# Performance work log

Measured on AMD Instinct MI355X. Metric: run time of the kernel, lower is better.

## Reference

```python
import jax, jax.numpy as jnp
import numpy as np

K = 4  # knn_graph(k=4, loop=False) hard-coded in H2GCN.forward


def _knn_2hop_adj(Fet, k):
    """Per-batch kNN graph -> symmetrize -> 2-hop binary adjacency [B,N,N].

    Matches create_adj + get_2hop_neighbors: edge direction and the row
    normalization in create_adj are irrelevant because get_2hop_neighbors
    symmetrizes (adj[row,col]=adj[col,row]=1) and thresholds (adj@adj > 0).
    """
    B, N, _ = Fet.shape
    sq = jnp.sum(Fet * Fet, axis=-1)  # [B,N]
    dist = sq[:, :, None] + sq[:, None, :] - 2.0 * jnp.einsum('bnf,bmf->bnm', Fet, Fet)
    eye = jnp.eye(N, dtype=bool)
    dist = jnp.where(eye[None], jnp.inf, dist)  # loop=False: exclude self
    _, idx = jax.lax.top_k(-dist, k)  # [B,N,k] nearest-neighbor indices
    b_idx = jnp.arange(B)[:, None, None]
    n_idx = jnp.arange(N)[None, :, None]
    A = jnp.zeros((B, N, N), Fet.dtype).at[b_idx, n_idx, idx].set(1.0)
    A = jnp.maximum(A, jnp.swapaxes(A, 1, 2))  # symmetrize 1-hop
    A2 = jnp.einsum('bnm,bmk->bnk', A, A)      # 2-hop counts
    A2 = jnp.where(eye[None], 0.0, A2)          # fill_diagonal_(0)
    return (A2 > 0).astype(Fet.dtype)


def _h2gcn_conv(x, A2, w1, b1, w2, b2):
    """H2GCNConv on dense binary adjacency.

    Dense matmul with binary A2 == gather(x[col]) -> fc2 -> index_add over rows;
    A2.sum(-1) == bincount(row). Degree clamped to >= 1.
    """
    ego = jnp.einsum('bnf,of->bno', x, w1) + b1   # fc1(x)
    msg = jnp.einsum('bnf,of->bno', x, w2) + b2   # fc2(x)
    agg = jnp.einsum('bnm,bmo->bno', A2, msg)     # scatter-add of neighbor msgs
    deg = jnp.maximum(jnp.sum(A2, axis=-1, keepdims=True), 1.0)
    return jax.nn.relu(jnp.concatenate([ego, agg / deg], axis=-1))


def setup_inputs() -> dict:
    key = jax.random.key(0)
    ks = jax.random.split(key, 8)
    B, N, F, NH, NC = 128, 197, 768, 512, 1000
    s = 0.02
    return {
        'Fet': jax.random.normal(ks[0], (B, N, F), jnp.float32),
        'w1_0': jax.random.normal(ks[1], (NH, F), jnp.float32) * s,
        'b1_0': jnp.zeros((NH,), jnp.float32),
        'w2_0': jax.random.normal(ks[2], (NH, F), jnp.float32) * s,
        'b2_0': jnp.zeros((NH,), jnp.float32),
        'w1_1': jax.random.normal(ks[3], (NH, 2 * NH), jnp.float32) * s,
        'b1_1': jnp.zeros((NH,), jnp.float32),
        'w2_1': jax.random.normal(ks[4], (NH, 2 * NH), jnp.float32) * s,
        'b2_1': jnp.zeros((NH,), jnp.float32),
        'fc1_w': jax.random.normal(ks[5], (NH, 4 * NH), jnp.float32) * s,
        'fc1_b': jnp.zeros((NH,), jnp.float32),
        'fc2_w': jax.random.normal(ks[6], (NC, NH), jnp.float32) * s,
        'fc2_b': jnp.zeros((NC,), jnp.float32),
    }


def reference(Fet, w1_0, b1_0, w2_0, b2_0, w1_1, b1_1, w2_1, b2_1,
              fc1_w, fc1_b, fc2_w, fc2_b):
    A2 = _knn_2hop_adj(Fet, K)
    h1 = _h2gcn_conv(Fet, A2, w1_0, b1_0, w2_0, b2_0)   # [B,N,2*nhid]
    h2 = _h2gcn_conv(h1, A2, w1_1, b1_1, w2_1, b2_1)    # [B,N,2*nhid]
    h = jnp.concatenate([h1, h2], axis=-1)              # [B,N,final_dim]
    graph_features = jnp.mean(h, axis=1)                # global_mean_pool
    p = jax.nn.relu(graph_features @ fc1_w.T + fc1_b)   # dropout is identity (eval)
    out = p @ fc2_w.T + fc2_b
    return (out, graph_features)
```

## Files before the change

kernel.cpp:

```cpp
#include <hip/hip_runtime.h>
#include <hip/hip_bf16.h>
#include <math.h>

typedef __attribute__((ext_vector_type(8))) short bf16x8;
typedef __attribute__((ext_vector_type(4))) float f32x4;

#define B_ 128
#define N_ 197
#define F_ 768
#define NH_ 512
#define D2_ 1024
#define D4_ 2048
#define NC_ 1000
#define ROWS_ (B_ * N_)
#define KA_ 224
#define NA_ 256

#define OFF_DIST0  0ull
#define OFF_SQ     19871232ull
#define OFF_ABITS  19972352ull
#define OFF_DEG    20779520ull
#define OFF_FETHI  20880640ull
#define OFF_MSGT   59710720ull
#define OFF_H1     89070848ull
#define OFF_FETLO  OFF_MSGT
#define OFF_POOL   140844288ull
#define OFF_P      141892864ull
#define OFF_WC1    142155008ull
#define OFF_WC2    143727872ull
#define OFF_DIST1  145825024ull

__device__ __forceinline__ void gll16(const void* g, void* l) {
  __builtin_amdgcn_global_load_lds((const __attribute__((address_space(1))) void*)g,
                                   (__attribute__((address_space(3))) void*)l, 16, 0, 0);
}

__device__ __forceinline__ int slot_of(int row) { return (row & 3) ^ ((row >> 2) & 3); }

__global__ __launch_bounds__(256) void cast_bf16_kernel(const float* __restrict__ src,
                                                        __hip_bfloat16* __restrict__ dst,
                                                        int n4) {
  int i = blockIdx.x * 256 + threadIdx.x;
  if (i >= n4) return;
  float4 v = ((const float4*)src)[i];
  union { __hip_bfloat16 h[4]; uint2 u; } pk;
  pk.h[0] = __float2bfloat16(v.x);
  pk.h[1] = __float2bfloat16(v.y);
  pk.h[2] = __float2bfloat16(v.z);
  pk.h[3] = __float2bfloat16(v.w);
  ((uint2*)dst)[i] = pk.u;
}

__global__ __launch_bounds__(256) void cast_hilo_sq(const float* __restrict__ X,
                                                    __hip_bfloat16* __restrict__ hi,
                                                    __hip_bfloat16* __restrict__ lo,
                                                    float* __restrict__ sq) {
  int row = blockIdx.x * 4 + (threadIdx.x >> 6);
  int lane = threadIdx.x & 63;
  const float4* xp = (const float4*)(X + (size_t)row * F_);
  uint2* hp = (uint2*)(hi + (size_t)row * F_);
  uint2* lp = (uint2*)(lo + (size_t)row * F_);
  float s = 0.f;
#pragma unroll
  for (int i = 0; i < 3; i++) {
    float4 v = xp[lane + i * 64];
    s += v.x * v.x + v.y * v.y + v.z * v.z + v.w * v.w;
    float f[4] = {v.x, v.y, v.z, v.w};
    union { __hip_bfloat16 h[4]; uint2 u; } ph, pl;
#pragma unroll
    for (int k = 0; k < 4; k++) {
      __hip_bfloat16 h = __float2bfloat16(f[k]);
      ph.h[k] = h;
      pl.h[k] = __float2bfloat16(f[k] - __bfloat162float(h));
    }
    hp[lane + i * 64] = ph.u;
    lp[lane + i * 64] = pl.u;
  }
#pragma unroll
  for (int o = 32; o > 0; o >>= 1) s += __shfl_down(s, o);
  if (lane == 0) sq[row] = s;
}

__global__ __launch_bounds__(256) void mfma_gram(const __hip_bfloat16* __restrict__ Xhi,
                                                 const __hip_bfloat16* __restrict__ Xlo,
                                                 float* __restrict__ g0,
                                                 float* __restrict__ g1) {
  __shared__ short AsH[4096];
  __shared__ short BsH[4096];
  __shared__ short AsL[4096];
  __shared__ short BsL[4096];
  const int t = threadIdx.x;
  const int wgid = blockIdx.x;
  const int L = (wgid & 7) * 96 + (wgid >> 3);
  const int b = L / 6;
  const int rbx = L - b * 6;
  const int bx = rbx % 3;
  const int khalf = rbx / 3;
  const int m0 = (bx == 0) ? 0 : 128;
  const int o0 = (bx == 2) ? 128 : 0;
  const bool mirror = (bx == 1);
  const int l = t & 63, w = t >> 6;
  const int wm = (w >> 1) * 64, wn = (w & 1) * 64;
  const int frow = l & 15, fch = l >> 4;
  const int srow = t >> 2, sslot = t & 3;
  const size_t rowbase = (size_t)b * N_;
  const char* AhiB = (const char*)(Xhi + (rowbase + m0) * F_);
  const char* AloB = (const char*)(Xlo + (rowbase + m0) * F_);
  const char* BhiB = (const char*)(Xhi + (rowbase + o0) * F_);
  const char* BloB = (const char*)(Xlo + (rowbase + o0) * F_);
  const int rb = F_ * 2;
  char* AsHB = (char*)AsH;
  char* BsHB = (char*)BsH;
  char* AsLB = (char*)AsL;
  char* BsLB = (char*)BsL;
  float* go = khalf ? g1 : g0;
  f32x4 zero = {0.f, 0.f, 0.f, 0.f};
  f32x4 acc[4][4];
#pragma unroll
  for (int i = 0; i < 4; i++)
#pragma unroll
    for (int j = 0; j < 4; j++) acc[i][j] = zero;
  const int kt0 = khalf * 12;
  for (int kt = kt0; kt < kt0 + 12; kt++) {
    const int kb = kt * 64;
#pragma unroll
    for (int u = 0; u < 2; u++) {
      int grow = u * 64 + srow;
      int gslot = sslot ^ slot_of(grow);
      size_t goff = (size_t)grow * rb + kb + gslot * 16;
      gll16(AhiB + goff, AsHB + u * 4096 + t * 16);
      gll16(BhiB + goff, BsHB + u * 4096 + t * 16);
      gll16(AloB + goff, AsLB + u * 4096 + t * 16);
      gll16(BloB + goff, BsLB + u * 4096 + t * 16);
    }
    __syncthreads();
    bf16x8 ah[4], al[4], bh[4], bl[4];
#pragma unroll
    for (int i = 0; i < 4; i++) {
      int ar = wm + i * 16 + frow;
      int aoff = ar * 64 + ((fch ^ slot_of(ar)) * 16);
      ah[i] = *(const bf16x8*)(AsHB + aoff);
      al[i] = *(const bf16x8*)(AsLB + aoff);
      int br = wn + i * 16 + frow;
      int boff = br * 64 + ((fch ^ slot_of(br)) * 16);
      bh[i] = *(const bf16x8*)(BsHB + boff);
      bl[i] = *(const bf16x8*)(BsLB + boff);
    }
#pragma unroll
    for (int i = 0; i < 4; i++)
#pragma unroll
      for (int j = 0; j < 4; j++) {
        acc[i][j] = __builtin_amdgcn_mfma_f32_16x16x32_bf16(ah[i], bh[j], acc[i][j], 0, 0, 0);
        acc[i][j] = __builtin_amdgcn_mfma_f32_16x16x32_bf16(ah[i], bl[j], acc[i][j], 0, 0, 0);
        acc[i][j] = __builtin_amdgcn_mfma_f32_16x16x32_bf16(al[i], bh[j], acc[i][j], 0, 0, 0);
      }
    __syncthreads();
  }
#pragma unroll
  for (int j = 0; j < 4; j++) {
    int m = o0 + wn + j * 16 + frow;
    if (m >= N_) continue;
#pragma unroll
    for (int i = 0; i < 4; i++) {
      int nb = m0 + wm + i * 16 + fch * 4;
#pragma unroll
      for (int r = 0; r < 4; r++) {
        int n = nb + r;
        if (n >= N_) continue;
        float g = acc[i][j][r];
        go[(rowbase + n) * N_ + m] = g;
        if (mirror) go[(rowbase + m) * N_ + n] = g;
      }
    }
  }
}

__global__ __launch_bounds__(256) void topk_kernel(const float* __restrict__ g0,
                                                   const float* __restrict__ g1,
                                                   const float* __restrict__ sq,
                                                   unsigned long long* __restrict__ Abits) {
  int row = blockIdx.x * 4 + (threadIdx.x >> 6);
  int lane = threadIdx.x & 63;
  int b = row / N_, n = row - b * N_;
  const float* g0r = g0 + (size_t)row * N_;
  const float* g1r = g1 + (size_t)row * N_;
  const float* sqb = sq + (size_t)b * N_;
  float v[4];
  int vi[4];
#pragma unroll
  for (int i = 0; i < 4; i++) {
    int m = lane + i * 64;
    bool ok = (m < N_) && (m != n);
    v[i] = ok ? (sqb[m] - 2.f * (g0r[m] + g1r[m])) : INFINITY;
    vi[i] = ok ? m : 0x3fffffff;
  }
  unsigned long long nbr[4] = {0ull, 0ull, 0ull, 0ull};
#pragma unroll
  for (int t = 0; t < 4; t++) {
    float bv = v[0];
    int bi = vi[0];
#pragma unroll
    for (int i = 1; i < 4; i++)
      if (v[i] < bv || (v[i] == bv && vi[i] < bi)) { bv = v[i]; bi = vi[i]; }
#pragma unroll
    for (int o = 1; o < 64; o <<= 1) {
      float ov = __shfl_xor(bv, o);
      int oi = __shfl_xor(bi, o);
      if (ov < bv || (ov == bv && oi < bi)) { bv = ov; bi = oi; }
    }
#pragma unroll
    for (int i = 0; i < 4; i++)
      if (vi[i] == bi) { v[i] = INFINITY; vi[i] = 0x3fffffff; }
    if (lane == 0) {
      nbr[bi >> 6] |= 1ull << (bi & 63);
      atomicOr(&Abits[((size_t)b * N_ + bi) * 4 + (n >> 6)], 1ull << (n & 63));
    }
  }
  if (lane == 0) {
#pragma unroll
    for (int w = 0; w < 4; w++)
      if (nbr[w]) atomicOr(&Abits[(size_t)row * 4 + w], nbr[w]);
  }
}

__global__ __launch_bounds__(256) void a2_kernel(const unsigned long long* __restrict__ Abits,
                                                 __hip_bfloat16* __restrict__ A2bf,
                                                 float* __restrict__ deg) {
  int row = blockIdx.x * 4 + (threadIdx.x >> 6);
  int lane = threadIdx.x & 63;
  int b = row / N_, n = row - b * N_;
  const unsigned long long* arow = Abits + (size_t)row * 4;
  const unsigned long long* base = Abits + (size_t)b * N_ * 4;
  unsigned long long r0 = 0, r1 = 0, r2 = 0, r3 = 0;
#pragma unroll
  for (int w = 0; w < 4; w++) {
    if ((arow[w] >> lane) & 1ull) {
      const unsigned long long* mr = base + (size_t)(w * 64 + lane) * 4;
      r0 |= mr[0]; r1 |= mr[1]; r2 |= mr[2]; r3 |= mr[3];
    }
  }
#pragma unroll
  for (int o = 1; o < 64; o <<= 1) {
    r0 |= __shfl_xor(r0, o);
    r1 |= __shfl_xor(r1, o);
    r2 |= __shfl_xor(r2, o);
    r3 |= __shfl_xor(r3, o);
  }
  unsigned long long rr[4] = {r0, r1, r2, r3};
  rr[n >> 6] &= ~(1ull << (n & 63));
  __hip_bfloat16* out = A2bf + ((size_t)b * NA_ + n) * KA_;
  const __hip_bfloat16 one = __float2bfloat16(1.f);
  const __hip_bfloat16 zer = __float2bfloat16(0.f);
#pragma unroll
  for (int i = 0; i < 4; i++) {
    int m = lane + i * 64;
    if (m < KA_)
      out[m] = (m < N_ && ((rr[m >> 6] >> (m & 63)) & 1ull)) ? one : zer;
  }
  if (lane == 0) {
    int dg = __popcll(rr[0]) + __popcll(rr[1]) + __popcll(rr[2]) + __popcll(rr[3]);
    deg[row] = (float)(dg > 0 ? dg : 1);
  }
}

template <int MODE>
__global__ __launch_bounds__(256) void mfma_fused(const __hip_bfloat16* __restrict__ X,
                                                  const __hip_bfloat16* __restrict__ Wcat,
                                                  const float* __restrict__ biasE,
                                                  const float* __restrict__ biasM,
                                                  __hip_bfloat16* __restrict__ h1,
                                                  __hip_bfloat16* __restrict__ msgT,
                                                  float* __restrict__ pool,
                                                  int K) {
  __shared__ short As[4096];
  __shared__ short Bs[4096];
  const int t = threadIdx.x;
  const int wgid = blockIdx.x;
  const int L = (wgid & 7) * 197 + (wgid >> 3);
  const int m0 = (L >> 3) * 128, o0 = (L & 7) * 128;
  const int l = t & 63, w = t >> 6;
  const int wm = (w >> 1) * 64, wn = (w & 1) * 64;
  const int frow = l & 15, fch = l >> 4;
  const int srow = t >> 2, sslot = t & 3;
  const char* Abase = (const char*)(X + (size_t)m0 * K);
  const char* Bbase = (const char*)(Wcat + (size_t)o0 * K);
  const int rb = K * 2;
  char* AsB = (char*)As;
  char* BsB = (char*)Bs;
  const bool swap = (o0 >= 512);
  f32x4 zero = {0.f, 0.f, 0.f, 0.f};
  f32x4 acc[4][4];
#pragma unroll
  for (int i = 0; i < 4; i++)
#pragma unroll
    for (int j = 0; j < 4; j++) acc[i][j] = zero;
  const int KT = K >> 5;
  for (int kt = 0; kt < KT; kt++) {
    const int kb = kt * 64;
#pragma unroll
    for (int u = 0; u < 2; u++) {
      int grow = u * 64 + srow;
      int gslot = sslot ^ slot_of(grow);
      gll16(Abase + (size_t)grow * rb + kb + gslot * 16, AsB + u * 4096 + t * 16);
      gll16(Bbase + (size_t)grow * rb + kb + gslot * 16, BsB + u * 4096 + t * 16);
    }
    __syncthreads();
    bf16x8 af[4], bfv[4];
#pragma unroll
    for (int i = 0; i < 4; i++) {
      int ar = wm + i * 16 + frow;
      af[i] = *(const bf16x8*)(AsB + ar * 64 + ((fch ^ slot_of(ar)) * 16));
      int br = wn + i * 16 + frow;
      bfv[i] = *(const bf16x8*)(BsB + br * 64 + ((fch ^ slot_of(br)) * 16));
    }
    if (!swap) {
#pragma unroll
      for (int i = 0; i < 4; i++)
#pragma unroll
        for (int j = 0; j < 4; j++)
          acc[i][j] = __builtin_amdgcn_mfma_f32_16x16x32_bf16(af[i], bfv[j], acc[i][j], 0, 0, 0);
    } else {
#pragma unroll
      for (int i = 0; i < 4; i++)
#pragma unroll
        for (int j = 0; j < 4; j++)
          acc[i][j] = __builtin_amdgcn_mfma_f32_16x16x32_bf16(bfv[j], af[i], acc[i][j], 0, 0, 0);
    }
    __syncthreads();
  }
  if (!swap) {
#pragma unroll
    for (int j = 0; j < 4; j++) {
      int c = o0 + wn + j * 16 + frow;
      float bv = biasE[c];
      if (MODE == 1) {
#pragma unroll
        for (int i = 0; i < 4; i++) {
          int r0 = m0 + wm + i * 16 + fch * 4;
#pragma unroll
          for (int r = 0; r < 4; r++) {
            float v = fmaxf(acc[i][j][r] + bv, 0.f);
            h1[(size_t)(r0 + r) * D2_ + c] = __float2bfloat16(v);
          }
        }
      } else {
        int rw = m0 + wm;
        int b0 = rw / N_;
        int rB = (b0 + 1) * N_;
        float sA = 0.f, sB = 0.f;
#pragma unroll
        for (int i = 0; i < 4; i++) {
          int r0 = m0 + wm + i * 16 + fch * 4;
#pragma unroll
          for (int r = 0; r < 4; r++) {
            float v = fmaxf(acc[i][j][r] + bv, 0.f);
            if (r0 + r < rB) sA += v; else sB += v;
          }
        }
        sA += __shfl_down(sA, 32);
        sA += __shfl_down(sA, 16);
        sB += __shfl_down(sB, 32);
        sB += __shfl_down(sB, 16);
        if (l < 16) {
          atomicAdd(&pool[(size_t)b0 * D4_ + D2_ + c], sA);
          if (rw + 64 > rB) atomicAdd(&pool[(size_t)(b0 + 1) * D4_ + D2_ + c], sB);
        }
      }
    }
  } else {
#pragma unroll
    for (int i = 0; i < 4; i++) {
      int xrow = m0 + wm + i * 16 + frow;
      int bb = xrow / N_;
      int rr = xrow - bb * N_;
      __hip_bfloat16* mt = msgT + (size_t)bb * NH_ * KA_ + rr;
#pragma unroll
      for (int j = 0; j < 4; j++) {
#pragma unroll
        for (int r = 0; r < 4; r++) {
          int cm = (o0 - 512) + wn + j * 16 + fch * 4 + r;
          float v = acc[i][j][r] + biasM[cm];
          mt[(size_t)cm * KA_] = __float2bfloat16(v);
        }
      }
    }
  }
}

template <int MODE>
__global__ __launch_bounds__(256) void mfma_agg(const __hip_bfloat16* __restrict__ A2bf,
                                                const __hip_bfloat16* __restrict__ msgT,
                                                const float* __restrict__ deg,
                                                __hip_bfloat16* __restrict__ H,
                                                float* __restrict__ pool, int poolOff) {
  __shared__ short As[4096];
  __shared__ short Bs[4096];
  const int t = threadIdx.x;
  const int wgid = blockIdx.x;
  const int L = (wgid & 7) * 128 + (wgid >> 3);
  const int b = L >> 3;
  const int o0 = ((L >> 1) & 3) * 128;
  const int m0 = (L & 1) * 128;
  const int l = t & 63, w = t >> 6;
  const int wm = (w >> 1) * 64, wn = (w & 1) * 64;
  const int frow = l & 15, fch = l >> 4;
  const int srow = t >> 2, sslot = t & 3;
  const char* Abase = (const char*)(A2bf + ((size_t)b * NA_ + m0) * KA_);
  const char* Bbase = (const char*)(msgT + ((size_t)b * NH_ + o0) * KA_);
  const int rb = KA_ * 2;
  char* AsB = (char*)As;
  char* BsB = (char*)Bs;
  f32x4 zero = {0.f, 0.f, 0.f, 0.f};
  f32x4 acc[4][4];
#pragma unroll
  for (int i = 0; i < 4; i++)
#pragma unroll
    for (int j = 0; j < 4; j++) acc[i][j] = zero;
  for (int kt = 0; kt < 7; kt++) {
    const int kb = kt * 64;
#pragma unroll
    for (int u = 0; u < 2; u++) {
      int grow = u * 64 + srow;
      int gslot = sslot ^ slot_of(grow);
      gll16(Abase + (size_t)grow * rb + kb + gslot * 16, AsB + u * 4096 + t * 16);
      gll16(Bbase + (size_t)grow * rb + kb + gslot * 16, BsB + u * 4096 + t * 16);
    }
    __syncthreads();
    bf16x8 af[4], bfv[4];
#pragma unroll
    for (int i = 0; i < 4; i++) {
      int ar = wm + i * 16 + frow;
      af[i] = *(const bf16x8*)(AsB + ar * 64 + ((fch ^ slot_of(ar)) * 16));
      int br = wn + i * 16 + frow;
      bfv[i] = *(const bf16x8*)(BsB + br * 64 + ((fch ^ slot_of(br)) * 16));
    }
#pragma unroll
    for (int i = 0; i < 4; i++)
#pragma unroll
      for (int j = 0; j < 4; j++)
        acc[i][j] = __builtin_amdgcn_mfma_f32_16x16x32_bf16(af[i], bfv[j], acc[i][j], 0, 0, 0);
    __syncthreads();
  }
#pragma unroll
  for (int j = 0; j < 4; j++) {
    int c = o0 + wn + j * 16 + frow;
    float s = 0.f;
#pragma unroll
    for (int i = 0; i < 4; i++) {
#pragma unroll
      for (int r = 0; r < 4; r++) {
        int n = m0 + wm + i * 16 + fch * 4 + r;
        if (n < N_) {
          float dv = deg[b * N_ + n];
          float v = fmaxf(acc[i][j][r] / dv, 0.f);
          if (MODE == 0)
            H[((size_t)b * N_ + n) * D2_ + NH_ + c] = __float2bfloat16(v);
          s += v;
        }
      }
    }
    s += __shfl_down(s, 32);
    s += __shfl_down(s, 16);
    if (l < 16) atomicAdd(&pool[(size_t)b * D4_ + poolOff + c], s);
  }
}

__global__ __launch_bounds__(256) void pool_h1ego(const __hip_bfloat16* __restrict__ h1,
                                                  float* __restrict__ gf) {
  int b = blockIdx.y;
  int c = blockIdx.x * 256 + threadIdx.x;
  const __hip_bfloat16* p = h1 + (size_t)b * N_ * D2_ + c;
  float s = 0.f;
  for (int n = 0; n < N_; n++) s += __bfloat162float(p[(size_t)n * D2_]);
  gf[(size_t)b * D4_ + c] = s * (1.f / N_);
}

__global__ __launch_bounds__(256) void scale_pool(const float* __restrict__ pool,
                                                  float* __restrict__ gf) {
  int b = blockIdx.y;
  int c = NH_ + blockIdx.x * 256 + threadIdx.x;
  gf[(size_t)b * D4_ + c] = pool[(size_t)b * D4_ + c] * (1.f / N_);
}

template <bool RELUX>
__global__ __launch_bounds__(256) void head_gemm(const float* __restrict__ Xg,
                                                 const float* __restrict__ W,
                                                 const float* __restrict__ bias,
                                                 float* __restrict__ Y,
                                                 int Rows, int Fin, int O, int kchunk) {
  __shared__ float Xs[16][68];
  __shared__ float Ws[16][68];
  int tx = threadIdx.x, ty = threadIdx.y;
  int tid = ty * 16 + tx;
  int lr = tid >> 2;
  int lk = (tid & 3) * 4;
  int rbase = blockIdx.y * 64;
  int o0 = blockIdx.x * 64;
  int k0base = blockIdx.z * kchunk;
  float acc[4][4] = {};
  for (int k0 = k0base; k0 < k0base + kchunk; k0 += 16) {
    float4 xv = make_float4(0.f, 0.f, 0.f, 0.f);
    if (rbase + lr < Rows) xv = *(const float4*)&Xg[(size_t)(rbase + lr) * Fin + k0 + lk];
    if (RELUX) {
      xv.x = fmaxf(xv.x, 0.f); xv.y = fmaxf(xv.y, 0.f);
      xv.z = fmaxf(xv.z, 0.f); xv.w = fmaxf(xv.w, 0.f);
    }
    Xs[lk][lr] = xv.x; Xs[lk + 1][lr] = xv.y; Xs[lk + 2][lr] = xv.z; Xs[lk + 3][lr] = xv.w;
    float4 wv = make_float4(0.f, 0.f, 0.f, 0.f);
    if (o0 + lr < O) wv = *(const float4*)&W[(size_t)(o0 + lr) * Fin + k0 + lk];
    Ws[lk][lr] = wv.x; Ws[lk + 1][lr] = wv.y; Ws[lk + 2][lr] = wv.z; Ws[lk + 3][lr] = wv.w;
    __syncthreads();
#pragma unroll
    for (int k = 0; k < 16; k++) {
      float4 a = *(const float4*)&Xs[k][ty * 4];
      float4 bb = *(const float4*)&Ws[k][tx * 4];
      float av[4] = {a.x, a.y, a.z, a.w};
      float bv[4] = {bb.x, bb.y, bb.z, bb.w};
#pragma unroll
      for (int i = 0; i < 4; i++)
#pragma unroll
        for (int j = 0; j < 4; j++) acc[i][j] = fmaf(av[i], bv[j], acc[i][j]);
    }
    __syncthreads();
  }
#pragma unroll
  for (int i = 0; i < 4; i++) {
    int rrow = rbase + ty * 4 + i;
    if (rrow >= Rows) continue;
#pragma unroll
    for (int j = 0; j < 4; j++) {
      int c = o0 + tx * 4 + j;
      if (c >= O) continue;
      float vv = acc[i][j] + ((blockIdx.z == 0) ? bias[c] : 0.f);
      atomicAdd(&Y[(size_t)rrow * O + c], vv);
    }
  }
}

extern "C" void kernel_launch(void* const* d_in, const int* in_sizes, int n_in,
                              void* d_out, int out_size, void* d_ws, size_t ws_size,
                              hipStream_t stream) {
  const float* Fet  = (const float*)d_in[0];
  const float* w1_0 = (const float*)d_in[1];
  const float* b1_0 = (const float*)d_in[2];
  const float* w2_0 = (const float*)d_in[3];
  const float* b2_0 = (const float*)d_in[4];
  const float* w1_1 = (const float*)d_in[5];
  const float* b1_1 = (const float*)d_in[6];
  const float* w2_1 = (const float*)d_in[7];
  const float* b2_1 = (const float*)d_in[8];
  const float* fc1_w = (const float*)d_in[9];
  const float* fc1_b = (const float*)d_in[10];
  const float* fc2_w = (const float*)d_in[11];
  const float* fc2_b = (const float*)d_in[12];

  char* ws = (char*)d_ws;
  float* g0 = (float*)(ws + OFF_DIST0);
  float* g1 = (float*)(ws + OFF_DIST1);
  __hip_bfloat16* A2bf = (__hip_bfloat16*)(ws + OFF_DIST0);
  float* sq = (float*)(ws + OFF_SQ);
  unsigned long long* Abits = (unsigned long long*)(ws + OFF_ABITS);
  float* deg = (float*)(ws + OFF_DEG);
  __hip_bfloat16* Fet_hi = (__hip_bfloat16*)(ws + OFF_FETHI);
  __hip_bfloat16* Fet_lo = (__hip_bfloat16*)(ws + OFF_FETLO);
  __hip_bfloat16* msgT = (__hip_bfloat16*)(ws + OFF_MSGT);
  __hip_bfloat16* h1 = (__hip_bfloat16*)(ws + OFF_H1);
  float* pool = (float*)(ws + OFF_POOL);
  float* p = (float*)(ws + OFF_P);
  __hip_bfloat16* wc1 = (__hip_bfloat16*)(ws + OFF_WC1);
  __hip_bfloat16* wc2 = (__hip_bfloat16*)(ws + OFF_WC2);

  float* out = (float*)d_out;
  float* gf = out + (size_t)B_ * NC_;

  hipMemsetAsync(Abits, 0, (size_t)ROWS_ * 4 * sizeof(unsigned long long), stream);
  hipMemsetAsync(pool, 0, (size_t)B_ * D4_ * sizeof(float), stream);
  hipMemsetAsync(p, 0, (size_t)B_ * NH_ * sizeof(float), stream);
  hipMemsetAsync(out, 0, (size_t)B_ * NC_ * sizeof(float), stream);

  cast_hilo_sq<<<ROWS_ / 4, 256, 0, stream>>>(Fet, Fet_hi, Fet_lo, sq);
  cast_bf16_kernel<<<384, 256, 0, stream>>>(w1_0, wc1, NH_ * F_ / 4);
  cast_bf16_kernel<<<384, 256, 0, stream>>>(w2_0, wc1 + (size_t)NH_ * F_, NH_ * F_ / 4);
  cast_bf16_kernel<<<512, 256, 0, stream>>>(w1_1, wc2, NH_ * D2_ / 4);
  cast_bf16_kernel<<<512, 256, 0, stream>>>(w2_1, wc2 + (size_t)NH_ * D2_, NH_ * D2_ / 4);

  mfma_gram<<<768, 256, 0, stream>>>(Fet_hi, Fet_lo, g0, g1);
  topk_kernel<<<ROWS_ / 4, 256, 0, stream>>>(g0, g1, sq, Abits);
  a2_kernel<<<ROWS_ / 4, 256, 0, stream>>>(Abits, A2bf, deg);

  mfma_fused<1><<<1576, 256, 0, stream>>>(Fet_hi, wc1, b1_0, b2_0, h1, msgT, nullptr, F_);
  mfma_agg<0><<<1024, 256, 0, stream>>>(A2bf, msgT, deg, h1, pool, NH_);

  mfma_fused<2><<<1576, 256, 0, stream>>>(h1, wc2, b1_1, b2_1, nullptr, msgT, pool, D2_);
  mfma_agg<1><<<1024, 256, 0, stream>>>(A2bf, msgT, deg, nullptr, pool, D2_ + NH_);

  pool_h1ego<<<dim3(2, B_), 256, 0, stream>>>(h1, gf);
  scale_pool<<<dim3(6, B_), 256, 0, stream>>>(pool, gf);

  head_gemm<false><<<dim3(8, 2, 16), dim3(16, 16), 0, stream>>>(
      gf, fc1_w, fc1_b, p, B_, D4_, NH_, 128);
  head_gemm<true><<<dim3(16, 2, 8), dim3(16, 16), 0, stream>>>(
      p, fc2_w, fc2_b, out, B_, NH_, NC_, 64);
}
```

Measured before the change: 525.2 us.

## Transpose MFMA outputs for vectorized stores and repack msgT layout per channel

Swaps the MFMA operand order in the gram, fused and aggregation GEMMs so each lane holds four consecutive columns. Epilogues can then write 4-wide vectors for h1, msgT and the gram rows, instead of strided scalar stores. msgT is relaid as [channel][batch*KA] with a per-batch pad offset mirrored in the A2 columns, the gram buffers get a padded row stride of 200, and the four weight cast launches are merged into one. Gains come from cheaper, coalesced epilogue stores and fewer launches. The cost is more involved indexing and pad bookkeeping, plus a pool reduction that now issues more atomics.

```diff
diff --git a/kernel.cpp b/kernel.cpp
--- a/kernel.cpp
+++ b/kernel.cpp
@@ -15,20 +15,22 @@
 #define ROWS_ (B_ * N_)
 #define KA_ 224
 #define NA_ 256
-
-#define OFF_DIST0  0ull
-#define OFF_SQ     19871232ull
-#define OFF_ABITS  19972352ull
-#define OFF_DEG    20779520ull
-#define OFF_FETHI  20880640ull
-#define OFF_MSGT   59710720ull
-#define OFF_H1     89070848ull
+#define LDG_ 200
+#define MT_LD_ (B_ * KA_)
+
+#define OFF_G0     0ull
+#define OFF_SQ     20172800ull
+#define OFF_ABITS  20273664ull
+#define OFF_DEG    21080576ull
+#define OFF_FETHI  21181440ull
+#define OFF_MSGT   60011520ull
+#define OFF_H1     89371648ull
 #define OFF_FETLO  OFF_MSGT
-#define OFF_POOL   140844288ull
-#define OFF_P      141892864ull
-#define OFF_WC1    142155008ull
-#define OFF_WC2    143727872ull
-#define OFF_DIST1  145825024ull
+#define OFF_POOL   141014016ull
+#define OFF_P      142062592ull
+#define OFF_WC1    142324736ull
+#define OFF_WC2    143897600ull
+#define OFF_G1     145994752ull
 
 __device__ __forceinline__ void gll16(const void* g, void* l) {
   __builtin_amdgcn_global_load_lds((const __attribute__((address_space(1))) void*)g,
@@ -37,18 +39,29 @@
 
 __device__ __forceinline__ int slot_of(int row) { return (row & 3) ^ ((row >> 2) & 3); }
 
-__global__ __launch_bounds__(256) void cast_bf16_kernel(const float* __restrict__ src,
-                                                        __hip_bfloat16* __restrict__ dst,
-                                                        int n4) {
+__global__ __launch_bounds__(256) void cast_weights(const float* __restrict__ w10,
+                                                    const float* __restrict__ w20,
+                                                    const float* __restrict__ w11,
+                                                    const float* __restrict__ w21,
+                                                    __hip_bfloat16* __restrict__ wc1,
+                                                    __hip_bfloat16* __restrict__ wc2) {
+  const int S1 = NH_ * F_ / 4;
+  const int S2 = NH_ * D2_ / 4;
   int i = blockIdx.x * 256 + threadIdx.x;
-  if (i >= n4) return;
-  float4 v = ((const float4*)src)[i];
+  const float* src;
+  __hip_bfloat16* dst;
+  int off;
+  if (i < S1) { src = w10; dst = wc1; off = i; }
+  else if (i < 2 * S1) { src = w20; dst = wc1 + (size_t)NH_ * F_; off = i - S1; }
+  else if (i < 2 * S1 + S2) { src = w11; dst = wc2; off = i - 2 * S1; }
+  else { src = w21; dst = wc2 + (size_t)NH_ * D2_; off = i - 2 * S1 - S2; }
+  float4 v = ((const float4*)src)[off];
   union { __hip_bfloat16 h[4]; uint2 u; } pk;
   pk.h[0] = __float2bfloat16(v.x);
   pk.h[1] = __float2bfloat16(v.y);
   pk.h[2] = __float2bfloat16(v.z);
   pk.h[3] = __float2bfloat16(v.w);
-  ((uint2*)dst)[i] = pk.u;
+  ((uint2*)dst)[off] = pk.u;
 }
 
 __global__ __launch_bounds__(256) void cast_hilo_sq(const float* __restrict__ X,
@@ -150,26 +163,27 @@
     for (int i = 0; i < 4; i++)
 #pragma unroll
       for (int j = 0; j < 4; j++) {
-        acc[i][j] = __builtin_amdgcn_mfma_f32_16x16x32_bf16(ah[i], bh[j], acc[i][j], 0, 0, 0);
-        acc[i][j] = __builtin_amdgcn_mfma_f32_16x16x32_bf16(ah[i], bl[j], acc[i][j], 0, 0, 0);
-        acc[i][j] = __builtin_amdgcn_mfma_f32_16x16x32_bf16(al[i], bh[j], acc[i][j], 0, 0, 0);
+        acc[i][j] = __builtin_amdgcn_mfma_f32_16x16x32_bf16(bh[j], ah[i], acc[i][j], 0, 0, 0);
+        acc[i][j] = __builtin_amdgcn_mfma_f32_16x16x32_bf16(bl[j], ah[i], acc[i][j], 0, 0, 0);
+        acc[i][j] = __builtin_amdgcn_mfma_f32_16x16x32_bf16(bh[j], al[i], acc[i][j], 0, 0, 0);
       }
     __syncthreads();
   }
 #pragma unroll
-  for (int j = 0; j < 4; j++) {
-    int m = o0 + wn + j * 16 + frow;
-    if (m >= N_) continue;
-#pragma unroll
-    for (int i = 0; i < 4; i++) {
-      int nb = m0 + wm + i * 16 + fch * 4;
-#pragma unroll
-      for (int r = 0; r < 4; r++) {
-        int n = nb + r;
-        if (n >= N_) continue;
-        float g = acc[i][j][r];
-        go[(rowbase + n) * N_ + m] = g;
-        if (mirror) go[(rowbase + m) * N_ + n] = g;
+  for (int i = 0; i < 4; i++) {
+    int n = m0 + wm + i * 16 + frow;
+    if (n >= N_) continue;
+    float* gr = go + (rowbase + n) * LDG_;
+#pragma unroll
+    for (int j = 0; j < 4; j++) {
+      int mb = o0 + wn + j * 16 + fch * 4;
+      if (mb >= LDG_) continue;
+      f32x4 pv = acc[i][j];
+      *(f32x4*)&gr[mb] = pv;
+      if (mirror) {
+#pragma unroll
+        for (int r = 0; r < 4; r++)
+          go[(rowbase + mb + r) * LDG_ + n] = pv[r];
       }
     }
   }
@@ -182,8 +196,8 @@
   int row = blockIdx.x * 4 + (threadIdx.x >> 6);
   int lane = threadIdx.x & 63;
   int b = row / N_, n = row - b * N_;
-  const float* g0r = g0 + (size_t)row * N_;
-  const float* g1r = g1 + (size_t)row * N_;
+  const float* g0r = g0 + (size_t)row * LDG_;
+  const float* g1r = g1 + (size_t)row * LDG_;
   const float* sqb = sq + (size_t)b * N_;
   float v[4];
   int vi[4];
@@ -248,14 +262,18 @@
   }
   unsigned long long rr[4] = {r0, r1, r2, r3};
   rr[n >> 6] &= ~(1ull << (n & 63));
+  const int pad = b & 3;
   __hip_bfloat16* out = A2bf + ((size_t)b * NA_ + n) * KA_;
   const __hip_bfloat16 one = __float2bfloat16(1.f);
   const __hip_bfloat16 zer = __float2bfloat16(0.f);
 #pragma unroll
   for (int i = 0; i < 4; i++) {
     int m = lane + i * 64;
-    if (m < KA_)
-      out[m] = (m < N_ && ((rr[m >> 6] >> (m & 63)) & 1ull)) ? one : zer;
+    if (m < KA_) {
+      int k = m - pad;
+      bool bit = (k >= 0 && k < N_ && ((rr[k >> 6] >> (k & 63)) & 1ull));
+      out[m] = bit ? one : zer;
+    }
   }
   if (lane == 0) {
     int dg = __popcll(rr[0]) + __popcll(rr[1]) + __popcll(rr[2]) + __popcll(rr[3]);
@@ -287,7 +305,8 @@
   const int rb = K * 2;
   char* AsB = (char*)As;
   char* BsB = (char*)Bs;
-  const bool swap = (o0 >= 512);
+  const bool ego = (o0 < 512);
+  const bool swap = (MODE == 1) && ego;
   f32x4 zero = {0.f, 0.f, 0.f, 0.f};
   f32x4 acc[4][4];
 #pragma unroll
@@ -328,22 +347,28 @@
     }
     __syncthreads();
   }
-  if (!swap) {
-#pragma unroll
-    for (int j = 0; j < 4; j++) {
-      int c = o0 + wn + j * 16 + frow;
-      float bv = biasE[c];
-      if (MODE == 1) {
+  if (ego) {
+    if (MODE == 1) {
+#pragma unroll
+      for (int j = 0; j < 4; j++) {
+        int c0 = o0 + wn + j * 16 + fch * 4;
+        float4 b4 = *(const float4*)&biasE[c0];
+        float bb4[4] = {b4.x, b4.y, b4.z, b4.w};
 #pragma unroll
         for (int i = 0; i < 4; i++) {
-          int r0 = m0 + wm + i * 16 + fch * 4;
-#pragma unroll
-          for (int r = 0; r < 4; r++) {
-            float v = fmaxf(acc[i][j][r] + bv, 0.f);
-            h1[(size_t)(r0 + r) * D2_ + c] = __float2bfloat16(v);
-          }
+          int xrow = m0 + wm + i * 16 + frow;
+          union { __hip_bfloat16 h[4]; uint2 u; } pk;
+#pragma unroll
+          for (int r = 0; r < 4; r++)
+            pk.h[r] = __float2bfloat16(fmaxf(acc[i][j][r] + bb4[r], 0.f));
+          *(uint2*)&h1[(size_t)xrow * D2_ + c0] = pk.u;
         }
-      } else {
+      }
+    } else {
+#pragma unroll
+      for (int j = 0; j < 4; j++) {
+        int c = o0 + wn + j * 16 + frow;
+        float bv = biasE[c];
         int rw = m0 + wm;
         int b0 = rw / N_;
         int rB = (b0 + 1) * N_;
@@ -369,18 +394,28 @@
     }
   } else {
 #pragma unroll
-    for (int i = 0; i < 4; i++) {
-      int xrow = m0 + wm + i * 16 + frow;
-      int bb = xrow / N_;
-      int rr = xrow - bb * N_;
-      __hip_bfloat16* mt = msgT + (size_t)bb * NH_ * KA_ + rr;
-#pragma unroll
-      for (int j = 0; j < 4; j++) {
-#pragma unroll
-        for (int r = 0; r < 4; r++) {
-          int cm = (o0 - 512) + wn + j * 16 + fch * 4 + r;
-          float v = acc[i][j][r] + biasM[cm];
-          mt[(size_t)cm * KA_] = __float2bfloat16(v);
+    for (int j = 0; j < 4; j++) {
+      int cm = (o0 - 512) + wn + j * 16 + frow;
+      float bm = biasM[cm];
+      __hip_bfloat16* mrow = msgT + (size_t)cm * MT_LD_;
+#pragma unroll
+      for (int i = 0; i < 4; i++) {
+        int x0 = m0 + wm + i * 16 + fch * 4;
+        int b0 = x0 / N_;
+        int r0 = x0 - b0 * N_;
+        union { __hip_bfloat16 h[4]; uint2 u; } pk;
+#pragma unroll
+        for (int r = 0; r < 4; r++) pk.h[r] = __float2bfloat16(acc[i][j][r] + bm);
+        if (r0 + 3 < N_) {
+          *(uint2*)&mrow[b0 * KA_ + (b0 & 3) + r0] = pk.u;
+        } else {
+#pragma unroll
+          for (int r = 0; r < 4; r++) {
+            int x = x0 + r;
+            int bb = x / N_;
+            int rx = x - bb * N_;
+            mrow[bb * KA_ + (bb & 3) + rx] = pk.h[r];
+          }
         }
       }
     }
@@ -391,7 +426,7 @@
 __global__ __launch_bounds__(256) void mfma_agg(const __hip_bfloat16* __restrict__ A2bf,
                                                 const __hip_bfloat16* __restrict__ msgT,
                                                 const float* __restrict__ deg,
-                                                __hip_bfloat16* __restrict__ H,
+                                                __hip_bfloat16* __restrict__ h1,
                                                 float* __restrict__ pool, int poolOff) {
   __shared__ short As[4096];
   __shared__ short Bs[4096];
@@ -406,8 +441,7 @@
   const int frow = l & 15, fch = l >> 4;
   const int srow = t >> 2, sslot = t & 3;
   const char* Abase = (const char*)(A2bf + ((size_t)b * NA_ + m0) * KA_);
-  const char* Bbase = (const char*)(msgT + ((size_t)b * NH_ + o0) * KA_);
-  const int rb = KA_ * 2;
+  const char* Bbase = (const char*)(msgT + (size_t)o0 * MT_LD_ + (size_t)b * KA_);
   char* AsB = (char*)As;
   char* BsB = (char*)Bs;
   f32x4 zero = {0.f, 0.f, 0.f, 0.f};
@@ -422,8 +456,8 @@
     for (int u = 0; u < 2; u++) {
       int grow = u * 64 + srow;
       int gslot = sslot ^ slot_of(grow);
-      gll16(Abase + (size_t)grow * rb + kb + gslot * 16, AsB + u * 4096 + t * 16);
-      gll16(Bbase + (size_t)grow * rb + kb + gslot * 16, BsB + u * 4096 + t * 16);
+      gll16(Abase + (size_t)grow * (KA_ * 2) + kb + gslot * 16, AsB + u * 4096 + t * 16);
+      gll16(Bbase + (size_t)grow * (MT_LD_ * 2) + kb + gslot * 16, BsB + u * 4096 + t * 16);
     }
     __syncthreads();
     bf16x8 af[4], bfv[4];
@@ -438,30 +472,45 @@
     for (int i = 0; i < 4; i++)
 #pragma unroll
       for (int j = 0; j < 4; j++)
-        acc[i][j] = __builtin_amdgcn_mfma_f32_16x16x32_bf16(af[i], bfv[j], acc[i][j], 0, 0, 0);
-    __syncthreads();
+        acc[i][j] = __builtin_amdgcn_mfma_f32_16x16x32_bf16(bfv[j], af[i], acc[i][j], 0, 0, 0);
+    __syncthreads();
+  }
+  float sv[4][4];
+#pragma unroll
+  for (int j = 0; j < 4; j++)
+#pragma unroll
+    for (int r = 0; r < 4; r++) sv[j][r] = 0.f;
+#pragma unroll
+  for (int i = 0; i < 4; i++) {
+    int n = m0 + wm + i * 16 + frow;
+    bool ok = (n < N_);
+    float dinv = ok ? (1.f / deg[b * N_ + n]) : 0.f;
+#pragma unroll
+    for (int j = 0; j < 4; j++) {
+      int c0 = o0 + wn + j * 16 + fch * 4;
+      union { __hip_bfloat16 h[4]; uint2 u; } pk;
+#pragma unroll
+      for (int r = 0; r < 4; r++) {
+        float v = ok ? fmaxf(acc[i][j][r] * dinv, 0.f) : 0.f;
+        sv[j][r] += v;
+        pk.h[r] = __float2bfloat16(v);
+      }
+      if (MODE == 0 && ok)
+        *(uint2*)&h1[((size_t)b * N_ + n) * D2_ + NH_ + c0] = pk.u;
+    }
   }
 #pragma unroll
   for (int j = 0; j < 4; j++) {
-    int c = o0 + wn + j * 16 + frow;
-    float s = 0.f;
-#pragma unroll
-    for (int i = 0; i < 4; i++) {
-#pragma unroll
-      for (int r = 0; r < 4; r++) {
-        int n = m0 + wm + i * 16 + fch * 4 + r;
-        if (n < N_) {
-          float dv = deg[b * N_ + n];
-          float v = fmaxf(acc[i][j][r] / dv, 0.f);
-          if (MODE == 0)
-            H[((size_t)b * N_ + n) * D2_ + NH_ + c] = __float2bfloat16(v);
-          s += v;
-        }
-      }
-    }
-    s += __shfl_down(s, 32);
-    s += __shfl_down(s, 16);
-    if (l < 16) atomicAdd(&pool[(size_t)b * D4_ + poolOff + c], s);
+#pragma unroll
+    for (int r = 0; r < 4; r++) {
+      float s = sv[j][r];
+      s += __shfl_down(s, 8, 16);
+      s += __shfl_down(s, 4, 16);
+      s += __shfl_down(s, 2, 16);
+      s += __shfl_down(s, 1, 16);
+      if ((l & 15) == 0)
+        atomicAdd(&pool[(size_t)b * D4_ + poolOff + o0 + wn + j * 16 + fch * 4 + r], s);
+    }
   }
 }
 
@@ -555,9 +604,9 @@
   const float* fc2_b = (const float*)d_in[12];
 
   char* ws = (char*)d_ws;
-  float* g0 = (float*)(ws + OFF_DIST0);
-  float* g1 = (float*)(ws + OFF_DIST1);
-  __hip_bfloat16* A2bf = (__hip_bfloat16*)(ws + OFF_DIST0);
+  float* g0 = (float*)(ws + OFF_G0);
+  float* g1 = (float*)(ws + OFF_G1);
+  __hip_bfloat16* A2bf = (__hip_bfloat16*)(ws + OFF_G0);
   float* sq = (float*)(ws + OFF_SQ);
   unsigned long long* Abits = (unsigned long long*)(ws + OFF_ABITS);
   float* deg = (float*)(ws + OFF_DEG);
@@ -579,10 +628,7 @@
   hipMemsetAsync(out, 0, (size_t)B_ * NC_ * sizeof(float), stream);
 
   cast_hilo_sq<<<ROWS_ / 4, 256, 0, stream>>>(Fet, Fet_hi, Fet_lo, sq);
-  cast_bf16_kernel<<<384, 256, 0, stream>>>(w1_0, wc1, NH_ * F_ / 4);
-  cast_bf16_kernel<<<384, 256, 0, stream>>>(w2_0, wc1 + (size_t)NH_ * F_, NH_ * F_ / 4);
-  cast_bf16_kernel<<<512, 256, 0, stream>>>(w1_1, wc2, NH_ * D2_ / 4);
-  cast_bf16_kernel<<<512, 256, 0, stream>>>(w2_1, wc2 + (size_t)NH_ * D2_, NH_ * D2_ / 4);
+  cast_weights<<<1792, 256, 0, stream>>>(w1_0, w2_0, w1_1, w2_1, wc1, wc2);
 
   mfma_gram<<<768, 256, 0, stream>>>(Fet_hi, Fet_lo, g0, g1);
   topk_kernel<<<ROWS_ / 4, 256, 0, stream>>>(g0, g1, sq, Abits);
```

Result: faster. 461.0 us (-12.2%).
